# Kernel tuning notes

Measured on AMD Instinct MI355X. Metric: run time of the kernel, lower is better.

The kernel has to match this reference:

```python
import jax, jax.numpy as jnp
import numpy as np

S = 1024      # MAX_SEQ_LEN
D_IN = 4096
H = 32        # num_heads
G = 8         # num_kv_groups
HD = 128      # head_dim
GS = H // G   # group_size


def _rope(t, cos, sin):
    # t: [heads, S, HD]; cos/sin: [S, HD]
    half = HD // 2
    t1, t2 = t[..., :half], t[..., half:]
    rotated = jnp.concatenate([-t2, t1], axis=-1)
    return t * cos[None] + rotated * sin[None]


def setup_inputs() -> dict:
    key = jax.random.key(0)
    ks = jax.random.split(key, 8)
    x = jax.random.normal(ks[0], (1, S, D_IN), dtype=jnp.float32)
    mask = jnp.triu(jnp.ones((S, S), dtype=bool), k=1)  # causal: True above diagonal
    # RoPE tables (standard llama frequencies)
    inv_freq = 1.0 / (10000.0 ** (jnp.arange(0, HD, 2, dtype=jnp.float32) / HD))
    angles = jnp.arange(S, dtype=jnp.float32)[:, None] * inv_freq[None, :]  # [S, HD/2]
    angles = jnp.concatenate([angles, angles], axis=-1)                     # [S, HD]
    cos, sin = jnp.cos(angles), jnp.sin(angles)
    sc = 0.02
    Wq = jax.random.normal(ks[1], (D_IN, H * HD), dtype=jnp.float32) * sc
    Wk = jax.random.normal(ks[2], (D_IN, G * HD), dtype=jnp.float32) * sc
    Wv = jax.random.normal(ks[3], (D_IN, G * HD), dtype=jnp.float32) * sc
    Wo = jax.random.normal(ks[4], (H * HD, D_IN), dtype=jnp.float32) * sc
    return {"x": x, "mask": mask, "cos": cos, "sin": sin,
            "Wq": Wq, "Wk": Wk, "Wv": Wv, "Wo": Wo}


def reference(x, mask, cos, sin, Wq, Wk, Wv, Wo):
    b, n_tok, _ = x.shape  # b == 1 (module squeezes dim 0)
    xs = x[0]                                        # [S, d_in]
    q = (xs @ Wq).reshape(n_tok, H, HD).transpose(1, 0, 2)   # [H, S, HD]
    k = (xs @ Wk).reshape(n_tok, G, HD).transpose(1, 0, 2)   # [G, S, HD]
    v = (xs @ Wv).reshape(n_tok, G, HD).transpose(1, 0, 2)   # [G, S, HD]
    q = _rope(q, cos, sin)
    k = _rope(k, cos, sin)
    # GQA expansion: repeat_interleave over head dim
    k = jnp.repeat(k, GS, axis=0)                    # [H, S, HD]
    v = jnp.repeat(v, GS, axis=0)
    scores = jnp.einsum('hsd,htd->hst', q, k)        # [H, S, S]
    scores = jnp.where(mask[None], -jnp.inf, scores) / jnp.sqrt(jnp.float32(HD))
    weights = jax.nn.softmax(scores, axis=-1)
    ctx = jnp.einsum('hst,htd->hsd', weights, v)     # [H, S, HD]
    ctx = ctx.transpose(1, 0, 2).reshape(n_tok, H * HD)
    out = ctx @ Wo                                   # [S, d_in]
    return out[None]                                 # [1, S, d_in]
```

## Files before the change

kernel.cpp:

```cpp
#include <hip/hip_runtime.h>
#include <hip/hip_bf16.h>

#define S_LEN 1024
#define DIN 4096
#define NH 32
#define NG 8
#define HD 128

typedef __bf16 bf16x8 __attribute__((ext_vector_type(8)));
typedef __bf16 bf16x4 __attribute__((ext_vector_type(4)));
typedef float f32x4 __attribute__((ext_vector_type(4)));

__device__ __forceinline__ void gload_lds16(const void* g, void* l) {
  __builtin_amdgcn_global_load_lds(
      (const __attribute__((address_space(1))) unsigned int*)g,
      (__attribute__((address_space(3))) unsigned int*)l, 16, 0, 0);
}

__device__ __forceinline__ unsigned pack2bf(float a, float b) {
  union { __bf16 h[2]; unsigned u; } x;
  x.h[0] = (__bf16)a; x.h[1] = (__bf16)b;
  return x.u;
}

__global__ __launch_bounds__(256) void k_cast(const float* __restrict__ in,
                                              __bf16* __restrict__ out, int n4) {
  int i = blockIdx.x * 256 + threadIdx.x;
  if (i >= n4) return;
  const float4 v = ((const float4*)in)[i];
  bf16x4 o;
  o.x = (__bf16)v.x; o.y = (__bf16)v.y; o.z = (__bf16)v.z; o.w = (__bf16)v.w;
  ((bf16x4*)out)[i] = o;
}

__global__ __launch_bounds__(256) void k_rope(__bf16* __restrict__ Q, __bf16* __restrict__ Kb,
                                              const float* __restrict__ cosT,
                                              const float* __restrict__ sinT) {
  int idx = blockIdx.x * 256 + threadIdx.x;
  const int QP = S_LEN * NH * 64;
  __bf16* t; int nh;
  if (idx < QP) { t = Q; nh = NH; }
  else {
    idx -= QP; t = Kb; nh = NG;
    if (idx >= S_LEN * NG * 64) return;
  }
  int d = idx & 63;
  int h = (idx >> 6) % nh;
  int s = idx / (64 * nh);
  float c = cosT[s * HD + d], sn = sinT[s * HD + d];
  size_t base = (size_t)s * nh * HD + h * HD + d;
  float t1 = (float)t[base], t2 = (float)t[base + 64];
  t[base]      = (__bf16)(t1 * c - t2 * sn);
  t[base + 64] = (__bf16)(t2 * c + t1 * sn);
}

template <int MODE>
__global__ __launch_bounds__(256, 3) void k_gemm(const __bf16* __restrict__ A,
                                                 const float* __restrict__ W0,
                                                 const float* __restrict__ W1,
                                                 const float* __restrict__ W2,
                                                 float* __restrict__ C,
                                                 __bf16* __restrict__ Qb,
                                                 __bf16* __restrict__ Kb,
                                                 __bf16* __restrict__ Vt) {
  __shared__ __bf16 As[2][128 * 64];
  __shared__ unsigned Bs[2][32 * 64];
  const int bm = blockIdx.y, bn = blockIdx.x;
  const int K = DIN, NT = K / 64;

  const float* Wsrc; int ldb, nloc;
  if (MODE == 0) { Wsrc = W0; ldb = 4096; nloc = bn * 64; }
  else {
    if (bn < 64)      { Wsrc = W0; ldb = 4096; nloc = bn * 64; }
    else if (bn < 80) { Wsrc = W1; ldb = 1024; nloc = (bn - 64) * 64; }
    else              { Wsrc = W2; ldb = 1024; nloc = (bn - 80) * 64; }
  }

  const int tid = threadIdx.x, w = tid >> 6;
  const int l = tid & 63, l15 = l & 15, g4 = l >> 4;

  f32x4 acc[2][4];
#pragma unroll
  for (int i = 0; i < 2; ++i)
#pragma unroll
    for (int j = 0; j < 4; ++j)
#pragma unroll
      for (int r = 0; r < 4; ++r) acc[i][j][r] = 0.f;

  float4 breg[2][2];

  auto issueB = [&](int t) {
#pragma unroll
    for (int p = 0; p < 2; ++p) {
      int c = p * 256 + tid;
      int kp = c >> 4, nn = (c & 15) * 4;
      const float* src = Wsrc + (size_t)(t * 64 + 2 * kp) * ldb + nloc + nn;
      breg[p][0] = *(const float4*)src;
      breg[p][1] = *(const float4*)(src + ldb);
    }
  };
  auto writeB = [&](int buf) {
#pragma unroll
    for (int p = 0; p < 2; ++p) {
      int c = p * 256 + tid;
      int kp = c >> 4, nn = (c & 15) * 4;
      int col = nn ^ (((kp >> 2) & 3) << 3);
      uint4 d;
      d.x = pack2bf(breg[p][0].x, breg[p][1].x);
      d.y = pack2bf(breg[p][0].y, breg[p][1].y);
      d.z = pack2bf(breg[p][0].z, breg[p][1].z);
      d.w = pack2bf(breg[p][0].w, breg[p][1].w);
      *(uint4*)&Bs[buf][kp * 64 + col] = d;
    }
  };
  auto issueA = [&](int t, int buf) {
    const __bf16* Ab = A + (size_t)(bm * 128) * K + t * 64;
#pragma unroll
    for (int p = 0; p < 4; ++p) {
      int c = p * 256 + tid;
      int row = c >> 3, gc = (c & 7) ^ (row & 7);
      gload_lds16(Ab + (size_t)row * K + gc * 8, &As[buf][(p * 256 + w * 64) * 8]);
    }
  };

  issueB(0);
  issueA(0, 0);
  writeB(0);
  __syncthreads();

  for (int t = 0; t < NT; ++t) {
    const int cur = t & 1;
    if (t + 1 < NT) {
      issueB(t + 1);
      issueA(t + 1, cur ^ 1);
    }
    bf16x8 af[2][2];
#pragma unroll
    for (int i = 0; i < 2; ++i) {
      int m = w * 32 + i * 16 + l15;
#pragma unroll
      for (int kk = 0; kk < 2; ++kk)
        af[i][kk] = *(const bf16x8*)((const char*)As[cur] + m * 128 + (((kk * 4 + g4) ^ (m & 7)) << 4));
    }
#pragma unroll
    for (int kk = 0; kk < 2; ++kk) {
      union { unsigned u[4]; bf16x8 v; } fb[4];
#pragma unroll
      for (int j = 0; j < 4; ++j) {
        const unsigned* bp = &Bs[cur][(kk * 16 + 4 * g4) * 64 + ((j * 16 + l15) ^ (g4 << 3))];
        fb[j].u[0] = bp[0];
        fb[j].u[1] = bp[64];
        fb[j].u[2] = bp[128];
        fb[j].u[3] = bp[192];
      }
#pragma unroll
      for (int i = 0; i < 2; ++i)
#pragma unroll
        for (int j = 0; j < 4; ++j)
          acc[i][j] = __builtin_amdgcn_mfma_f32_16x16x32_bf16(af[i][kk], fb[j].v, acc[i][j], 0, 0, 0);
    }
    if (t + 1 < NT) {
      writeB(cur ^ 1);
      __syncthreads();
    }
  }

  if constexpr (MODE == 0) {
#pragma unroll
    for (int i = 0; i < 2; ++i)
#pragma unroll
      for (int j = 0; j < 4; ++j)
#pragma unroll
        for (int r = 0; r < 4; ++r) {
          size_t row = bm * 128 + w * 32 + i * 16 + g4 * 4 + r;
          size_t col = bn * 64 + j * 16 + l15;
          C[row * 4096 + col] = acc[i][j][r];
        }
  } else {
    if (bn < 80) {
      __bf16* dst = (bn < 64) ? Qb : Kb;
      int ldc = (bn < 64) ? 4096 : 1024;
#pragma unroll
      for (int i = 0; i < 2; ++i)
#pragma unroll
        for (int j = 0; j < 4; ++j)
#pragma unroll
          for (int r = 0; r < 4; ++r) {
            size_t row = bm * 128 + w * 32 + i * 16 + g4 * 4 + r;
            size_t col = nloc + j * 16 + l15;
            dst[row * ldc + col] = (__bf16)acc[i][j][r];
          }
    } else {
#pragma unroll
      for (int i = 0; i < 2; ++i)
#pragma unroll
        for (int j = 0; j < 4; ++j) {
          size_t n = nloc + j * 16 + l15;
          size_t m0 = bm * 128 + w * 32 + i * 16 + g4 * 4;
          bf16x4 v;
          v.x = (__bf16)acc[i][j][0]; v.y = (__bf16)acc[i][j][1];
          v.z = (__bf16)acc[i][j][2]; v.w = (__bf16)acc[i][j][3];
          *(bf16x4*)&Vt[n * 1024 + m0] = v;
        }
    }
  }
}

__global__ __launch_bounds__(256) void k_attn(const __bf16* __restrict__ Q,
                                              const __bf16* __restrict__ Kb,
                                              const __bf16* __restrict__ Vt,
                                              __bf16* __restrict__ ctx) {
  __shared__ __align__(16) char lds_raw[65536];
  __bf16* Ks = (__bf16*)lds_raw;
  __bf16* Vs = (__bf16*)(lds_raw + 32768);

  const int h = blockIdx.y, g = h >> 2;
  const int q0 = blockIdx.x * 64;
  const int tid = threadIdx.x, w = tid >> 6, l = tid & 63;
  const int l15 = l & 15, g4 = l >> 4;
  const float scale = 0.08838834764831845f;

  bf16x8 qf[4];
  const int qrow = q0 + w * 16 + l15;
#pragma unroll
  for (int ks = 0; ks < 4; ++ks)
    qf[ks] = *(const bf16x8*)&Q[(size_t)qrow * (NH * HD) + h * HD + ks * 32 + g4 * 8];

  f32x4 acc[8];
#pragma unroll
  for (int i = 0; i < 8; ++i)
#pragma unroll
    for (int r = 0; r < 4; ++r) acc[i][r] = 0.f;
  float m_run = -__builtin_inff(), l_run = 0.f;

  const int ntiles = (q0 + 64 + 127) >> 7;
  for (int kt = 0; kt < ntiles; ++kt) {
    const int kv0 = kt * 128;
#pragma unroll
    for (int p = 0; p < 8; ++p) {
      int c = p * 256 + tid;
      int row = c >> 4, cc = c & 15;
      gload_lds16(&Kb[(size_t)(kv0 + row) * (NG * HD) + g * HD + ((cc ^ (row & 7)) << 3)],
                  &Ks[(p * 256 + w * 64) * 8]);
      gload_lds16(&Vt[(size_t)(g * HD + row) * S_LEN + kv0 + ((cc ^ (row & 7)) << 3)],
                  &Vs[(p * 256 + w * 64) * 8]);
    }
    __syncthreads();

    float sreg[8][4];
    const bool need_mask = (kv0 + 127 > q0);
#pragma unroll
    for (int tf = 0; tf < 8; ++tf) {
      f32x4 sa;
#pragma unroll
      for (int r = 0; r < 4; ++r) sa[r] = 0.f;
      int t_loc = tf * 16 + l15;
#pragma unroll
      for (int ks = 0; ks < 4; ++ks) {
        bf16x8 kf = *(const bf16x8*)((const char*)Ks + t_loc * 256 + (((ks * 4 + g4) ^ (t_loc & 7)) << 4));
        sa = __builtin_amdgcn_mfma_f32_16x16x32_bf16(kf, qf[ks], sa, 0, 0, 0);
      }
#pragma unroll
      for (int r = 0; r < 4; ++r) {
        float v = sa[r] * scale;
        if (need_mask && (kv0 + tf * 16 + g4 * 4 + r) > qrow) v = -__builtin_inff();
        sreg[tf][r] = v;
      }
    }
    float mx = -__builtin_inff();
#pragma unroll
    for (int tf = 0; tf < 8; ++tf)
#pragma unroll
      for (int r = 0; r < 4; ++r) mx = fmaxf(mx, sreg[tf][r]);
    mx = fmaxf(mx, __shfl_xor(mx, 16));
    mx = fmaxf(mx, __shfl_xor(mx, 32));
    const float m_new = fmaxf(m_run, mx);
    const float alpha = __expf(m_run - m_new);
    float ssum = 0.f;
#pragma unroll
    for (int tf = 0; tf < 8; ++tf)
#pragma unroll
      for (int r = 0; r < 4; ++r) {
        sreg[tf][r] = __expf(sreg[tf][r] - m_new);
        ssum += sreg[tf][r];
      }
    ssum += __shfl_xor(ssum, 16);
    ssum += __shfl_xor(ssum, 32);
    l_run = l_run * alpha + ssum;
    m_run = m_new;
    float ar[4];
#pragma unroll
    for (int r = 0; r < 4; ++r) ar[r] = __shfl(alpha, g4 * 4 + r);
#pragma unroll
    for (int nf = 0; nf < 8; ++nf)
#pragma unroll
      for (int r = 0; r < 4; ++r) acc[nf][r] *= ar[r];

    __syncthreads();

    char* pb = lds_raw + w * 4096;
#pragma unroll
    for (int tf = 0; tf < 8; ++tf) {
      int chunkc = 2 * tf + (g4 >> 1);
      int addr = l15 * 256 + ((chunkc ^ (l15 & 7)) << 4) + ((g4 & 1) << 3);
      *(unsigned*)(pb + addr)     = pack2bf(sreg[tf][0], sreg[tf][1]);
      *(unsigned*)(pb + addr + 4) = pack2bf(sreg[tf][2], sreg[tf][3]);
    }
    asm volatile("s_waitcnt lgkmcnt(0)" ::: "memory");
    bf16x8 pf[4];
#pragma unroll
    for (int ks = 0; ks < 4; ++ks)
      pf[ks] = *(const bf16x8*)(pb + l15 * 256 + (((ks * 4 + g4) ^ (l15 & 7)) << 4));
#pragma unroll
    for (int nf = 0; nf < 8; ++nf) {
      int d_loc = nf * 16 + l15;
#pragma unroll
      for (int ks = 0; ks < 4; ++ks) {
        bf16x8 vf = *(const bf16x8*)((const char*)Vs + d_loc * 256 + (((ks * 4 + g4) ^ (d_loc & 7)) << 4));
        acc[nf] = __builtin_amdgcn_mfma_f32_16x16x32_bf16(pf[ks], vf, acc[nf], 0, 0, 0);
      }
    }
    __syncthreads();
  }
  float li[4];
#pragma unroll
  for (int r = 0; r < 4; ++r) li[r] = 1.f / __shfl(l_run, g4 * 4 + r);
#pragma unroll
  for (int nf = 0; nf < 8; ++nf)
#pragma unroll
    for (int r = 0; r < 4; ++r) {
      size_t row = q0 + w * 16 + g4 * 4 + r;
      size_t col = (size_t)h * HD + nf * 16 + l15;
      ctx[row * (NH * HD) + col] = (__bf16)(acc[nf][r] * li[r]);
    }
}

extern "C" void kernel_launch(void* const* d_in, const int* in_sizes, int n_in,
                              void* d_out, int out_size, void* d_ws, size_t ws_size,
                              hipStream_t stream) {
  const float* x    = (const float*)d_in[0];
  const float* cosT = (const float*)d_in[2];
  const float* sinT = (const float*)d_in[3];
  const float* Wq   = (const float*)d_in[4];
  const float* Wk   = (const float*)d_in[5];
  const float* Wv   = (const float*)d_in[6];
  const float* Wo   = (const float*)d_in[7];
  float* out = (float*)d_out;

  char* ws = (char*)d_ws;
  const size_t MB = 1u << 20;
  __bf16* xb   = (__bf16*)(ws + 0);
  __bf16* Qb   = (__bf16*)(ws + 8 * MB);
  __bf16* Kbuf = (__bf16*)(ws + 16 * MB);
  __bf16* Vtb  = (__bf16*)(ws + 18 * MB);
  __bf16* ctxb = (__bf16*)(ws + 0);

  k_cast<<<4096, 256, 0, stream>>>(x, xb, (S_LEN * DIN) / 4);

  k_gemm<1><<<dim3(96, 8), 256, 0, stream>>>(xb, Wq, Wk, Wv, nullptr, Qb, Kbuf, Vtb);

  k_rope<<<10240, 256, 0, stream>>>(Qb, Kbuf, cosT, sinT);

  k_attn<<<dim3(16, 32), 256, 0, stream>>>(Qb, Kbuf, Vtb, ctxb);

  k_gemm<0><<<dim3(64, 8), 256, 0, stream>>>(ctxb, Wo, nullptr, nullptr, out,
                                             nullptr, nullptr, nullptr);
}
```

Before: 228.6 us.

## Load fp32 weights directly to LDS and drop GEMM double buffering

The GEMM main loop now brings the fp32 weight tile straight into shared memory with global_load_lds, where before it went through registers and was packed to bf16 on the way in. Each fragment is converted to bf16 when it is read from LDS for the MFMA. The double-buffered A/B pipeline is replaced by a single buffer with two barriers per K-step, which cuts register and LDS staging work. In exchange, loads are no longer overlapped with compute, the fp32 tile doubles LDS traffic for B, and conversions are repeated for every fragment read.

After: 250.1 us. 9.4% more time.

```diff
diff --git a/kernel.cpp b/kernel.cpp
--- a/kernel.cpp
+++ b/kernel.cpp
@@ -63,8 +63,8 @@
                                                  __bf16* __restrict__ Qb,
                                                  __bf16* __restrict__ Kb,
                                                  __bf16* __restrict__ Vt) {
-  __shared__ __bf16 As[2][128 * 64];
-  __shared__ unsigned Bs[2][32 * 64];
+  __shared__ __bf16 As[128 * 64];
+  __shared__ float Bf[64 * 64];
   const int bm = blockIdx.y, bn = blockIdx.x;
   const int K = DIN, NT = K / 64;
 
@@ -87,82 +87,49 @@
 #pragma unroll
       for (int r = 0; r < 4; ++r) acc[i][j][r] = 0.f;
 
-  float4 breg[2][2];
-
-  auto issueB = [&](int t) {
-#pragma unroll
-    for (int p = 0; p < 2; ++p) {
-      int c = p * 256 + tid;
-      int kp = c >> 4, nn = (c & 15) * 4;
-      const float* src = Wsrc + (size_t)(t * 64 + 2 * kp) * ldb + nloc + nn;
-      breg[p][0] = *(const float4*)src;
-      breg[p][1] = *(const float4*)(src + ldb);
-    }
-  };
-  auto writeB = [&](int buf) {
-#pragma unroll
-    for (int p = 0; p < 2; ++p) {
-      int c = p * 256 + tid;
-      int kp = c >> 4, nn = (c & 15) * 4;
-      int col = nn ^ (((kp >> 2) & 3) << 3);
-      uint4 d;
-      d.x = pack2bf(breg[p][0].x, breg[p][1].x);
-      d.y = pack2bf(breg[p][0].y, breg[p][1].y);
-      d.z = pack2bf(breg[p][0].z, breg[p][1].z);
-      d.w = pack2bf(breg[p][0].w, breg[p][1].w);
-      *(uint4*)&Bs[buf][kp * 64 + col] = d;
-    }
-  };
-  auto issueA = [&](int t, int buf) {
+  for (int t = 0; t < NT; ++t) {
     const __bf16* Ab = A + (size_t)(bm * 128) * K + t * 64;
 #pragma unroll
     for (int p = 0; p < 4; ++p) {
       int c = p * 256 + tid;
       int row = c >> 3, gc = (c & 7) ^ (row & 7);
-      gload_lds16(Ab + (size_t)row * K + gc * 8, &As[buf][(p * 256 + w * 64) * 8]);
-    }
-  };
-
-  issueB(0);
-  issueA(0, 0);
-  writeB(0);
-  __syncthreads();
-
-  for (int t = 0; t < NT; ++t) {
-    const int cur = t & 1;
-    if (t + 1 < NT) {
-      issueB(t + 1);
-      issueA(t + 1, cur ^ 1);
-    }
+      gload_lds16(Ab + (size_t)row * K + gc * 8, &As[(p * 256 + w * 64) * 8]);
+    }
+    const float* Wb = Wsrc + (size_t)(t * 64) * ldb + nloc;
+#pragma unroll
+    for (int p = 0; p < 4; ++p) {
+      int c = p * 256 + tid;
+      int row = c >> 4, q = c & 15;
+      int gq = q ^ (((row >> 3) & 3) << 1);
+      gload_lds16(Wb + (size_t)row * ldb + gq * 4, &Bf[(p * 256 + w * 64) * 4]);
+    }
+    __syncthreads();
+
     bf16x8 af[2][2];
 #pragma unroll
     for (int i = 0; i < 2; ++i) {
       int m = w * 32 + i * 16 + l15;
 #pragma unroll
       for (int kk = 0; kk < 2; ++kk)
-        af[i][kk] = *(const bf16x8*)((const char*)As[cur] + m * 128 + (((kk * 4 + g4) ^ (m & 7)) << 4));
+        af[i][kk] = *(const bf16x8*)((const char*)As + m * 128 + (((kk * 4 + g4) ^ (m & 7)) << 4));
     }
 #pragma unroll
     for (int kk = 0; kk < 2; ++kk) {
-      union { unsigned u[4]; bf16x8 v; } fb[4];
 #pragma unroll
       for (int j = 0; j < 4; ++j) {
-        const unsigned* bp = &Bs[cur][(kk * 16 + 4 * g4) * 64 + ((j * 16 + l15) ^ (g4 << 3))];
-        fb[j].u[0] = bp[0];
-        fb[j].u[1] = bp[64];
-        fb[j].u[2] = bp[128];
-        fb[j].u[3] = bp[192];
-      }
-#pragma unroll
-      for (int i = 0; i < 2; ++i)
-#pragma unroll
-        for (int j = 0; j < 4; ++j)
-          acc[i][j] = __builtin_amdgcn_mfma_f32_16x16x32_bf16(af[i][kk], fb[j].v, acc[i][j], 0, 0, 0);
-    }
-    if (t + 1 < NT) {
-      writeB(cur ^ 1);
-      __syncthreads();
-    }
+        const float* bp = &Bf[(kk * 32 + g4 * 8) * 64 + ((j * 16 + l15) ^ (g4 << 3))];
+        bf16x8 bfrag;
+#pragma unroll
+        for (int d = 0; d < 4; ++d) {
+          bfrag[2 * d]     = (__bf16)bp[d * 128];
+          bfrag[2 * d + 1] = (__bf16)bp[d * 128 + 64];
+        }
+#pragma unroll
+        for (int i = 0; i < 2; ++i)
+          acc[i][j] = __builtin_amdgcn_mfma_f32_16x16x32_bf16(af[i][kk], bfrag, acc[i][j], 0, 0, 0);
+      }
+    }
+    __syncthreads();
   }
 
   if constexpr (MODE == 0) {
```
